# Kernel optimization log

Hardware: AMD Instinct MI355X
Metric: run time of the kernel (lower is better)

Reference implementation:

```python
import jax, jax.numpy as jnp
import numpy as np

N_HEAD = 8
N_QP = 4  # query/key points per head
N_VP = 4  # value points per head
D_SPH = 16  # scalar dims per head
SCALE_SCALAR = D_SPH ** (-0.5)
SCALE_POINT = (4.5 * N_QP) ** (-0.5)
SCALE_TOTAL = 3.0 ** (-0.5)  # scalar + pair bias + point logits


def _euclid(xp, r, t):
    # xp: (b,n,l,p,3), r: (b,l,3,3), t: (b,l,3)  -> row-vector convention: x @ r + t
    return jnp.einsum('bnlpk,blkc->bnlpc', xp, r) + t[:, None, :, None, :]


def _inv_euclid(xp, r, t):
    # (x - t) @ r^T
    return jnp.einsum('bnlpk,blck->bnlpc', xp - t[:, None, :, None, :], r)


def setup_inputs() -> dict:
    key = jax.random.key(0)
    ks = jax.random.split(key, 16)
    b, l, d_res, d_pair = 2, 512, 384, 128
    w = lambda k, shp, fan: jax.random.normal(k, shp, jnp.float32) * (fan ** -0.5)
    return {
        'x': jax.random.normal(ks[0], (b, l, d_res), jnp.float32),
        'e': jax.random.normal(ks[1], (b, l, l, d_pair), jnp.float32),
        'r': jax.random.normal(ks[2], (b, l, 3, 3), jnp.float32),
        't': jax.random.normal(ks[3], (b, l, 3), jnp.float32),
        'Wq_s': w(ks[4], (d_res, N_HEAD * D_SPH), d_res),
        'Wk_s': w(ks[5], (d_res, N_HEAD * D_SPH), d_res),
        'Wv_s': w(ks[6], (d_res, N_HEAD * D_SPH), d_res),
        'Wpb': w(ks[7], (d_pair, N_HEAD), d_pair),
        'Wq_p': w(ks[8], (d_res, N_HEAD * N_QP * 3), d_res),
        'Wk_p': w(ks[9], (d_res, N_HEAD * N_QP * 3), d_res),
        'Wv_p': w(ks[10], (d_res, N_HEAD * N_VP * 3), d_res),
        'gamma': jnp.log(jnp.expm1(jnp.ones((N_HEAD,), jnp.float32))),
        'Wout': w(ks[11], (N_HEAD * D_SPH + N_HEAD * d_pair + N_HEAD * N_VP * 3 + N_HEAD * N_VP, d_res), 1280),
        'bout': jnp.zeros((d_res,), jnp.float32),
    }


def reference(x, e, r, t, Wq_s, Wk_s, Wv_s, Wpb, Wq_p, Wk_p, Wv_p, gamma, Wout, bout):
    b, l, _ = x.shape
    n = N_HEAD

    def split_heads(v):  # (b,l,n*d) -> (b,n,l,d)
        return v.reshape(b, l, n, -1).transpose(0, 2, 1, 3)

    def split_points(v, p):  # (b,l,n*p*3) -> (b,n,l,p,3)
        return v.reshape(b, l, n, p, 3).transpose(0, 2, 1, 3, 4)

    q_s, k_s, v_s = (split_heads(x @ W) for W in (Wq_s, Wk_s, Wv_s))
    q_p = _euclid(split_points(x @ Wq_p, N_QP), r, t)
    k_p = _euclid(split_points(x @ Wk_p, N_QP), r, t)
    v_p = _euclid(split_points(x @ Wv_p, N_VP), r, t)

    logit_scalar = jnp.einsum('bnid,bnjd->bnij', q_s, k_s) * SCALE_SCALAR
    bias_pair = (e @ Wpb).transpose(0, 3, 1, 2)  # (b,n,i,j)
    # pairwise squared point distances, summed over points p and coords c
    diff = q_p[:, :, :, None] - k_p[:, :, None]  # (b,n,i,j,p,3)
    sqdist = (diff ** 2).sum(axis=(-1, -2))      # (b,n,i,j)
    logit_point = -0.5 * SCALE_POINT * gamma[None, :, None, None] * sqdist

    attn = jax.nn.softmax(SCALE_TOTAL * (logit_scalar + bias_pair + logit_point), axis=-1)

    out_scalar = jnp.einsum('bnij,bnjd->bnid', attn, v_s).transpose(0, 2, 1, 3).reshape(b, l, -1)
    out_pair = jnp.einsum('bnij,bijd->bnid', attn, e).transpose(0, 2, 1, 3).reshape(b, l, -1)
    out_point = jnp.einsum('bnij,bnjpc->bnipc', attn, v_p)
    out_point = _inv_euclid(out_point, r, t)  # (b,n,i,p,3)
    out_point_norm = jnp.sqrt((out_point ** 2).sum(-1))  # (b,n,i,p)
    out_point = out_point.transpose(0, 2, 1, 3, 4).reshape(b, l, -1)
    out_point_norm = out_point_norm.transpose(0, 2, 1, 3).reshape(b, l, -1)

    out = jnp.concatenate([out_scalar, out_pair, out_point, out_point_norm], axis=-1)
    return out @ Wout + bout
```

## Files before the change

kernel.cpp:

```cpp
#include <hip/hip_runtime.h>
#include <hip/hip_bf16.h>
#include <math.h>

#define NH 8
#define L 512
#define DP 128
#define DS 16
#define DCAT 1280
#define TJ 32
#define NCHUNK 4
#define CJ 128
#define PSTRIDE 1280

#define SCALE_SCALAR 0.25f
#define SCALE_POINT  0.23570226039551584f
#define SCALE_TOTAL  0.5773502691896258f

typedef __bf16 bf16_t;
typedef bf16_t bf16x8 __attribute__((ext_vector_type(8)));
typedef float  f32x4v __attribute__((ext_vector_type(4)));

__global__ __launch_bounds__(256) void k_pack(
    const float* __restrict__ x,
    const float* __restrict__ Wq_s, const float* __restrict__ Wk_s, const float* __restrict__ Wv_s,
    const float* __restrict__ Wq_p, const float* __restrict__ Wk_p, const float* __restrict__ Wv_p,
    __hip_bfloat16* __restrict__ xb, __hip_bfloat16* __restrict__ WallT) {
    int idx = blockIdx.x * 256 + threadIdx.x;
    const int T1 = 1024 * 384;
    if (idx < T1) {
        xb[idx] = __float2bfloat16(x[idx]);
    } else {
        int j = idx - T1;
        int n = j / 384, k = j % 384;
        float v;
        if      (n < 128) v = Wq_s[k * 128 + n];
        else if (n < 256) v = Wk_s[k * 128 + (n - 128)];
        else if (n < 384) v = Wv_s[k * 128 + (n - 256)];
        else if (n < 480) v = Wq_p[k * 96  + (n - 384)];
        else if (n < 576) v = Wk_p[k * 96  + (n - 480)];
        else              v = Wv_p[k * 96  + (n - 576)];
        WallT[(size_t)n * 384 + k] = __float2bfloat16(v);
    }
}

__global__ __launch_bounds__(256) void k_prep(const float* __restrict__ Wout,
                                              __hip_bfloat16* __restrict__ WoutT) {
    __shared__ float tile[64][65];
    const int tid = threadIdx.x;
    const int k0 = blockIdx.x * 64;
    const int n0 = blockIdx.y * 64;
#pragma unroll
    for (int s = 0; s < 16; ++s) {
        int idx = s * 256 + tid, kk = idx >> 6, nn = idx & 63;
        tile[kk][nn] = Wout[(size_t)(k0 + kk) * 384 + n0 + nn];
    }
    __syncthreads();
#pragma unroll
    for (int s = 0; s < 16; ++s) {
        int idx = s * 256 + tid, nn = idx >> 6, kk = idx & 63;
        WoutT[(size_t)(n0 + nn) * 1280 + k0 + kk] = __float2bfloat16(tile[kk][nn]);
    }
}

__global__ __launch_bounds__(256) void k_projm(
    const __hip_bfloat16* __restrict__ xb, const __hip_bfloat16* __restrict__ WallT,
    float* __restrict__ q_s, float* __restrict__ k_s, float* __restrict__ v_s,
    float* __restrict__ praw) {
    __shared__ __align__(16) bf16_t As[64 * 40];
    __shared__ __align__(16) bf16_t Bs[48 * 40];
    const int tid = threadIdx.x;
    const int row0 = blockIdx.x * 64, col0 = blockIdx.y * 48;
    const int w = tid >> 6, lane = tid & 63;
    f32x4v acc[3] = {};

    for (int k0 = 0; k0 < 384; k0 += 32) {
        __syncthreads();
        {
            int rr = tid >> 2, q = tid & 3;
            *reinterpret_cast<int4*>(&As[rr * 40 + q * 8]) =
                *reinterpret_cast<const int4*>(&xb[(size_t)(row0 + rr) * 384 + k0 + q * 8]);
            if (tid < 192)
                *reinterpret_cast<int4*>(&Bs[rr * 40 + q * 8]) =
                    *reinterpret_cast<const int4*>(&WallT[(size_t)(col0 + rr) * 384 + k0 + q * 8]);
        }
        __syncthreads();
        const int m = lane & 15, kq = lane >> 4;
        bf16x8 af = *reinterpret_cast<const bf16x8*>(&As[(w * 16 + m) * 40 + kq * 8]);
#pragma unroll
        for (int c = 0; c < 3; ++c) {
            bf16x8 bfr = *reinterpret_cast<const bf16x8*>(&Bs[(c * 16 + m) * 40 + kq * 8]);
            acc[c] = __builtin_amdgcn_mfma_f32_16x16x32_bf16(af, bfr, acc[c], 0, 0, 0);
        }
    }
    const int colL = lane & 15, rbase = (lane >> 4) * 4;
#pragma unroll
    for (int c = 0; c < 3; ++c) {
        int col = col0 + c * 16 + colL;
#pragma unroll
        for (int rg = 0; rg < 4; ++rg) {
            int row = row0 + w * 16 + rbase + rg;
            float v = acc[c][rg];
            int bb = row >> 9, ll = row & 511;
            if (col < 384) {
                int kind = col >> 7, n = (col >> 4) & 7, d = col & 15;
                float* dst = (kind == 0) ? q_s : (kind == 1) ? k_s : v_s;
                dst[((size_t)(bb * NH + n) * L + ll) * DS + d] = v;
            } else {
                praw[(size_t)row * 288 + (col - 384)] = v;
            }
        }
    }
}

__global__ __launch_bounds__(256) void k_euclid(
    const float* __restrict__ praw, const float* __restrict__ r, const float* __restrict__ t,
    float* __restrict__ q_p, float* __restrict__ k_p, float* __restrict__ v_p) {
    int idx = blockIdx.x * 256 + threadIdx.x;
    int row = idx / 288, o = idx % 288;
    int arr = o / 96, oo = o % 96;
    int n = oo / 12, pc = oo % 12, p = pc / 3, c = pc % 3;
    const float* base = praw + (size_t)row * 288 + arr * 96 + n * 12 + p * 3;
    float acc = t[row * 3 + c];
#pragma unroll
    for (int k = 0; k < 3; ++k) acc += base[k] * r[row * 9 + k * 3 + c];
    float* dst = (arr == 0) ? q_p : (arr == 1) ? k_p : v_p;
    int bb = row >> 9, ll = row & 511;
    dst[((size_t)(bb * NH + n) * L + ll) * 12 + pc] = acc;
}

__global__ __launch_bounds__(256) void k_attn(
    const float* __restrict__ e, const float* __restrict__ Wpb, const float* __restrict__ gamma,
    const float* __restrict__ q_s, const float* __restrict__ k_s, const float* __restrict__ v_s,
    const float* __restrict__ q_p, const float* __restrict__ k_p, const float* __restrict__ v_p,
    float* __restrict__ part) {
    __shared__ __align__(16) float et[TJ * DP];
    __shared__ __align__(16) float wpbT[NH * DP];
    __shared__ float pt[NH][36];
    __shared__ float ptT[TJ][NH];
    __shared__ __align__(16) float qsl[NH * 16];
    __shared__ __align__(16) float qpl[NH * 12];
    __shared__ float gsh[NH];

    const int tid = threadIdx.x;
    const int blk = blockIdx.x;
    const int bi = blk >> 2, chunk = blk & 3;
    const int b = bi >> 9, i = bi & 511, b8 = b * NH;
    const int nH = tid >> 5, jL = tid & 31;
    const int d4 = tid & 31, jsub = tid >> 5;

    for (int idx = tid; idx < NH * DP; idx += 256)
        wpbT[(idx >> 7) * DP + (idx & 127)] = Wpb[(idx & 127) * NH + (idx >> 7)];
    if (tid < 128) {
        int n = tid >> 4, d = tid & 15;
        qsl[n * 16 + d] = q_s[((size_t)(b8 + n) * L + i) * DS + d];
    } else if (tid < 224) {
        int o = tid - 128, n = o / 12, pc = o % 12;
        qpl[n * 12 + pc] = q_p[((size_t)(b8 + n) * L + i) * 12 + pc];
    } else if (tid < 232) {
        gsh[tid - 224] = gamma[tid - 224];
    }

    const int nS = tid >> 4, dS = tid & 15;
    const int oP = tid - 128;
    const int nP = (oP >= 0 && oP < 96) ? oP / 12 : 0;
    const int pcP = (oP >= 0 && oP < 96) ? oP % 12 : 0;
    const float* vsp = v_s + (((size_t)(b8 + nS) * L + chunk * CJ) << 4) + dS;
    const float* vpp = v_p + ((size_t)(b8 + nP) * L + chunk * CJ) * 12 + pcP;

    float lsum = 0.f;
    float4 accPair[NH];
#pragma unroll
    for (int n = 0; n < NH; ++n) accPair[n] = make_float4(0.f, 0.f, 0.f, 0.f);
    float accS = 0.f, accP = 0.f;

    const float4* esrc4 = reinterpret_cast<const float4*>(
        e + ((size_t)(b * L + i) * L + chunk * CJ) * DP);

    for (int tile = 0; tile < CJ / TJ; ++tile) {
        const int j0 = tile * TJ;
        __syncthreads();
#pragma unroll
        for (int s = 0; s < 4; ++s) {
            int idx = tid + s * 256;
            int j = idx >> 5, g = idx & 31;
            float4 v = esrc4[(size_t)(j0 + j) * 32 + g];
            reinterpret_cast<float4*>(et)[j * 32 + (g ^ j)] = v;
        }
        __syncthreads();
        {
            const int jg = chunk * CJ + j0 + jL;
            const float4* row4 = reinterpret_cast<const float4*>(et) + jL * 32;
            const float4* wr4 = reinterpret_cast<const float4*>(&wpbT[nH * DP]);
            float bsum = 0.f;
#pragma unroll 8
            for (int g = 0; g < 32; ++g) {
                float4 ev = row4[g ^ jL];
                float4 wv4 = wr4[g];
                bsum += ev.x * wv4.x + ev.y * wv4.y + ev.z * wv4.z + ev.w * wv4.w;
            }
            const float4* ksr = reinterpret_cast<const float4*>(k_s + (((size_t)(b8 + nH) * L + jg) << 4));
            const float4* q4 = reinterpret_cast<const float4*>(&qsl[nH * 16]);
            float ssum = 0.f;
#pragma unroll
            for (int g = 0; g < 4; ++g) {
                float4 kv = ksr[g], qv = q4[g];
                ssum += kv.x * qv.x + kv.y * qv.y + kv.z * qv.z + kv.w * qv.w;
            }
            const float4* kpr = reinterpret_cast<const float4*>(k_p + ((size_t)(b8 + nH) * L + jg) * 12);
            const float4* qp4 = reinterpret_cast<const float4*>(&qpl[nH * 12]);
            float sq = 0.f;
#pragma unroll
            for (int g = 0; g < 3; ++g) {
                float4 kv = kpr[g], qv = qp4[g];
                float d0;
                d0 = qv.x - kv.x; sq += d0 * d0;  d0 = qv.y - kv.y; sq += d0 * d0;
                d0 = qv.z - kv.z; sq += d0 * d0;  d0 = qv.w - kv.w; sq += d0 * d0;
            }
            float lg = SCALE_TOTAL * (ssum * SCALE_SCALAR + bsum
                                      - 0.5f * SCALE_POINT * gsh[nH] * sq);
            float pv = __expf(lg);
            lsum += pv;
            pt[nH][jL] = pv;
            ptT[jL][nH] = pv;
        }
        __syncthreads();
        {
            const float4* et4 = reinterpret_cast<const float4*>(et);
#pragma unroll
            for (int s = 0; s < 4; ++s) {
                int j = jsub * 4 + s;
                float4 ev = et4[j * 32 + (d4 ^ j)];
                const float4* pb4 = reinterpret_cast<const float4*>(&ptT[j][0]);
                float4 pA = pb4[0], pB = pb4[1];
#define ACCP(nn, ps) accPair[nn].x += (ps) * ev.x; accPair[nn].y += (ps) * ev.y; \
                     accPair[nn].z += (ps) * ev.z; accPair[nn].w += (ps) * ev.w;
                ACCP(0, pA.x) ACCP(1, pA.y) ACCP(2, pA.z) ACCP(3, pA.w)
                ACCP(4, pB.x) ACCP(5, pB.y) ACCP(6, pB.z) ACCP(7, pB.w)
#undef ACCP
            }
        }
        if (tid < 128) {
            const float* vp = vsp + (size_t)j0 * 16;
#pragma unroll
            for (int q = 0; q < 8; ++q) {
                float4 p4 = *reinterpret_cast<const float4*>(&pt[nS][q * 4]);
                accS += p4.x * vp[(q * 4 + 0) * 16] + p4.y * vp[(q * 4 + 1) * 16]
                      + p4.z * vp[(q * 4 + 2) * 16] + p4.w * vp[(q * 4 + 3) * 16];
            }
        } else if (tid < 224) {
            const float* vp = vpp + (size_t)j0 * 12;
#pragma unroll
            for (int q = 0; q < 8; ++q) {
                float4 p4 = *reinterpret_cast<const float4*>(&pt[nP][q * 4]);
                accP += p4.x * vp[(q * 4 + 0) * 12] + p4.y * vp[(q * 4 + 1) * 12]
                      + p4.z * vp[(q * 4 + 2) * 12] + p4.w * vp[(q * 4 + 3) * 12];
            }
        }
    }

    float* prow = part + (size_t)blk * PSTRIDE;
    lsum += __shfl_xor(lsum, 1);  lsum += __shfl_xor(lsum, 2);
    lsum += __shfl_xor(lsum, 4);  lsum += __shfl_xor(lsum, 8);
    lsum += __shfl_xor(lsum, 16);
    if (jL == 0) prow[1248 + nH] = lsum;
    if (tid < 128) prow[1024 + tid] = accS;
    else if (tid < 224) prow[1152 + (tid - 128)] = accP;

    float4* red4 = reinterpret_cast<float4*>(et);
    __syncthreads();
    if (jsub >= 4) {
#pragma unroll
        for (int n = 0; n < NH; ++n) red4[((jsub - 4) * NH + n) * 32 + d4] = accPair[n];
    }
    __syncthreads();
    if (jsub < 4) {
#pragma unroll
        for (int n = 0; n < NH; ++n) {
            float4 o = red4[(jsub * NH + n) * 32 + d4];
            accPair[n].x += o.x; accPair[n].y += o.y; accPair[n].z += o.z; accPair[n].w += o.w;
        }
    }
    __syncthreads();
    if (jsub == 2 || jsub == 3) {
#pragma unroll
        for (int n = 0; n < NH; ++n) red4[((jsub - 2) * NH + n) * 32 + d4] = accPair[n];
    }
    __syncthreads();
    if (jsub < 2) {
#pragma unroll
        for (int n = 0; n < NH; ++n) {
            float4 o = red4[(jsub * NH + n) * 32 + d4];
            accPair[n].x += o.x; accPair[n].y += o.y; accPair[n].z += o.z; accPair[n].w += o.w;
        }
    }
    __syncthreads();
    if (jsub == 1) {
#pragma unroll
        for (int n = 0; n < NH; ++n) red4[n * 32 + d4] = accPair[n];
    }
    __syncthreads();
    if (jsub == 0) {
#pragma unroll
        for (int n = 0; n < NH; ++n) {
            float4 o = red4[n * 32 + d4];
            accPair[n].x += o.x; accPair[n].y += o.y; accPair[n].z += o.z; accPair[n].w += o.w;
            *reinterpret_cast<float4*>(&prow[n * 128 + d4 * 4]) = accPair[n];
        }
    }
}

__global__ __launch_bounds__(256) void k_comb(
    const float* __restrict__ part, const float* __restrict__ r, const float* __restrict__ t,
    __hip_bfloat16* __restrict__ concat) {
    __shared__ float comb[1256];
    __shared__ float rtsh[12], osh[96], o2sh[96];
    const int tid = threadIdx.x;
    const int bi = blockIdx.x;
    const float* base = part + (size_t)bi * NCHUNK * PSTRIDE;
#pragma unroll
    for (int s = 0; s < 5; ++s) {
        int idx = tid + s * 256;
        if (idx < 1256)
            comb[idx] = base[idx] + base[PSTRIDE + idx] + base[2 * PSTRIDE + idx] + base[3 * PSTRIDE + idx];
    }
    if (tid >= 244 && tid < 256) {
        int c = tid - 244;
        rtsh[c] = (c < 9) ? r[bi * 9 + c] : t[bi * 3 + (c - 9)];
    }
    __syncthreads();
    __hip_bfloat16* crow = concat + (size_t)bi * DCAT;
    if (tid < 128) crow[tid] = __float2bfloat16(comb[1024 + tid] / comb[1248 + (tid >> 4)]);
    for (int idx = tid; idx < 1024; idx += 256)
        crow[128 + idx] = __float2bfloat16(comb[idx] / comb[1248 + (idx >> 7)]);
    if (tid >= 128 && tid < 224) {
        int o = tid - 128;
        osh[o] = comb[1152 + o] / comb[1248 + o / 12];
    }
    __syncthreads();
    if (tid < 96) {
        int n = tid / 12, pc = tid % 12, p = pc / 3, c = pc % 3;
        float oc = 0.f;
#pragma unroll
        for (int k = 0; k < 3; ++k)
            oc += (osh[n * 12 + p * 3 + k] - rtsh[9 + k]) * rtsh[c * 3 + k];
        crow[1152 + tid] = __float2bfloat16(oc);
        o2sh[tid] = oc;
    }
    __syncthreads();
    if (tid < 32) {
        int n = tid >> 2, p = tid & 3;
        float vx = o2sh[n * 12 + p * 3], vy = o2sh[n * 12 + p * 3 + 1], vz = o2sh[n * 12 + p * 3 + 2];
        crow[1248 + tid] = __float2bfloat16(sqrtf(vx * vx + vy * vy + vz * vz));
    }
}

__global__ __launch_bounds__(256) void k_out(const __hip_bfloat16* __restrict__ A,
                                             const __hip_bfloat16* __restrict__ Bt,
                                             const float* __restrict__ bout,
                                             float* __restrict__ out) {
    __shared__ __align__(16) bf16_t At[64 * 40];
    __shared__ __align__(16) bf16_t Bs[64 * 40];
    const int tid = threadIdx.x;
    const int row0 = blockIdx.x * 64, col0 = blockIdx.y * 64;
    const int wv = tid >> 6, lane = tid & 63;
    f32x4v acc[4] = {};

    for (int k0 = 0; k0 < 1280; k0 += 32) {
        __syncthreads();
        {
            int rr = tid >> 2, q = tid & 3;
            *reinterpret_cast<int4*>(&At[rr * 40 + q * 8]) =
                *reinterpret_cast<const int4*>(&A[(size_t)(row0 + rr) * 1280 + k0 + q * 8]);
            *reinterpret_cast<int4*>(&Bs[rr * 40 + q * 8]) =
                *reinterpret_cast<const int4*>(&Bt[(size_t)(col0 + rr) * 1280 + k0 + q * 8]);
        }
        __syncthreads();
        const int m = lane & 15, kq = lane >> 4;
        bf16x8 af = *reinterpret_cast<const bf16x8*>(&At[(wv * 16 + m) * 40 + kq * 8]);
#pragma unroll
        for (int nt = 0; nt < 4; ++nt) {
            bf16x8 bfr = *reinterpret_cast<const bf16x8*>(&Bs[(nt * 16 + m) * 40 + kq * 8]);
            acc[nt] = __builtin_amdgcn_mfma_f32_16x16x32_bf16(af, bfr, acc[nt], 0, 0, 0);
        }
    }
    const int col_l = lane & 15, rbase = (lane >> 4) * 4;
#pragma unroll
    for (int nt = 0; nt < 4; ++nt) {
        int col = col0 + nt * 16 + col_l;
        float bo = bout[col];
#pragma unroll
        for (int rg = 0; rg < 4; ++rg) {
            int rowg = row0 + wv * 16 + rbase + rg;
            out[(size_t)rowg * 384 + col] = acc[nt][rg] + bo;
        }
    }
}

extern "C" void kernel_launch(void* const* d_in, const int* in_sizes, int n_in,
                              void* d_out, int out_size, void* d_ws, size_t ws_size,
                              hipStream_t stream) {
    const float* x     = (const float*)d_in[0];
    const float* e     = (const float*)d_in[1];
    const float* r     = (const float*)d_in[2];
    const float* t     = (const float*)d_in[3];
    const float* Wq_s  = (const float*)d_in[4];
    const float* Wk_s  = (const float*)d_in[5];
    const float* Wv_s  = (const float*)d_in[6];
    const float* Wpb   = (const float*)d_in[7];
    const float* Wq_p  = (const float*)d_in[8];
    const float* Wk_p  = (const float*)d_in[9];
    const float* Wv_p  = (const float*)d_in[10];
    const float* gamma = (const float*)d_in[11];
    const float* Wout  = (const float*)d_in[12];
    const float* bout  = (const float*)d_in[13];

    float* ws   = (float*)d_ws;
    float* q_s  = ws + 0;
    float* k_s  = ws + 131072;
    float* v_s  = ws + 262144;
    float* q_p  = ws + 393216;
    float* k_p  = ws + 491520;
    float* v_p  = ws + 589824;
    float* praw = ws + 688128;
    __hip_bfloat16* xb     = (__hip_bfloat16*)((char*)d_ws + 3932160);
    __hip_bfloat16* WallT  = (__hip_bfloat16*)((char*)d_ws + 4718592);
    __hip_bfloat16* concat = (__hip_bfloat16*)((char*)d_ws + 5234688);
    __hip_bfloat16* WoutT  = (__hip_bfloat16*)((char*)d_ws + 7856128);
    float* part = (float*)((char*)d_ws + 8847360);
    float* out = (float*)d_out;

    hipLaunchKernelGGL(k_pack, dim3(2544), dim3(256), 0, stream,
                       x, Wq_s, Wk_s, Wv_s, Wq_p, Wk_p, Wv_p, xb, WallT);
    hipLaunchKernelGGL(k_prep, dim3(20, 6), dim3(256), 0, stream, Wout, WoutT);
    hipLaunchKernelGGL(k_projm, dim3(16, 14), dim3(256), 0, stream,
                       xb, WallT, q_s, k_s, v_s, praw);
    hipLaunchKernelGGL(k_euclid, dim3(1152), dim3(256), 0, stream,
                       praw, r, t, q_p, k_p, v_p);
    hipLaunchKernelGGL(k_attn, dim3(4096), dim3(256), 0, stream,
                       e, Wpb, gamma, q_s, k_s, v_s, q_p, k_p, v_p, part);
    hipLaunchKernelGGL(k_comb, dim3(1024), dim3(256), 0, stream,
                       part, r, t, concat);
    hipLaunchKernelGGL(k_out, dim3(16, 6), dim3(256), 0, stream, concat, WoutT, bout, out);
}
```

Measured before the change: 485.7 us.

## Use bf16 MFMA for pair bias and pair aggregation in attention kernel

Rewrites the attention kernel so the e·Wpb pair-bias projection and the attn·e pair aggregation run on 16x16x32 bf16 MFMA instructions. The e tile is converted to bf16 and stored both row-major and transposed in shared memory. The next e tile is prefetched into registers, and V scalars and points are read from new transposed bf16 copies written by the projection kernels. This removes the scalar FMA loops and the multi-stage shared-memory reduction of the pair accumulators, at the cost of bf16 precision on e, the probabilities and V, plus extra transposed writes.

```diff
diff --git a/kernel.cpp b/kernel.cpp
--- a/kernel.cpp
+++ b/kernel.cpp
@@ -18,6 +18,7 @@
 
 typedef __bf16 bf16_t;
 typedef bf16_t bf16x8 __attribute__((ext_vector_type(8)));
+typedef bf16_t bf16x4 __attribute__((ext_vector_type(4)));
 typedef float  f32x4v __attribute__((ext_vector_type(4)));
 
 __global__ __launch_bounds__(256) void k_pack(
@@ -65,7 +66,7 @@
 __global__ __launch_bounds__(256) void k_projm(
     const __hip_bfloat16* __restrict__ xb, const __hip_bfloat16* __restrict__ WallT,
     float* __restrict__ q_s, float* __restrict__ k_s, float* __restrict__ v_s,
-    float* __restrict__ praw) {
+    float* __restrict__ praw, __hip_bfloat16* __restrict__ v_sT) {
     __shared__ __align__(16) bf16_t As[64 * 40];
     __shared__ __align__(16) bf16_t Bs[48 * 40];
     const int tid = threadIdx.x;
@@ -105,6 +106,8 @@
                 int kind = col >> 7, n = (col >> 4) & 7, d = col & 15;
                 float* dst = (kind == 0) ? q_s : (kind == 1) ? k_s : v_s;
                 dst[((size_t)(bb * NH + n) * L + ll) * DS + d] = v;
+                if (kind == 2)
+                    v_sT[((size_t)((bb * NH + n) * DS + d)) * L + ll] = __float2bfloat16(v);
             } else {
                 praw[(size_t)row * 288 + (col - 384)] = v;
             }
@@ -114,7 +117,8 @@
 
 __global__ __launch_bounds__(256) void k_euclid(
     const float* __restrict__ praw, const float* __restrict__ r, const float* __restrict__ t,
-    float* __restrict__ q_p, float* __restrict__ k_p, float* __restrict__ v_p) {
+    float* __restrict__ q_p, float* __restrict__ k_p, float* __restrict__ v_p,
+    __hip_bfloat16* __restrict__ v_pT) {
     int idx = blockIdx.x * 256 + threadIdx.x;
     int row = idx / 288, o = idx % 288;
     int arr = o / 96, oo = o % 96;
@@ -126,30 +130,32 @@
     float* dst = (arr == 0) ? q_p : (arr == 1) ? k_p : v_p;
     int bb = row >> 9, ll = row & 511;
     dst[((size_t)(bb * NH + n) * L + ll) * 12 + pc] = acc;
-}
-
-__global__ __launch_bounds__(256) void k_attn(
+    if (arr == 2)
+        v_pT[((size_t)((bb * NH + n) * 12 + pc)) * L + ll] = __float2bfloat16(acc);
+}
+
+__global__ __launch_bounds__(256, 4) void k_attn(
     const float* __restrict__ e, const float* __restrict__ Wpb, const float* __restrict__ gamma,
-    const float* __restrict__ q_s, const float* __restrict__ k_s, const float* __restrict__ v_s,
-    const float* __restrict__ q_p, const float* __restrict__ k_p, const float* __restrict__ v_p,
+    const float* __restrict__ q_s, const float* __restrict__ k_s,
+    const float* __restrict__ q_p, const float* __restrict__ k_p,
+    const __hip_bfloat16* __restrict__ v_sT, const __hip_bfloat16* __restrict__ v_pT,
     float* __restrict__ part) {
-    __shared__ __align__(16) float et[TJ * DP];
-    __shared__ __align__(16) float wpbT[NH * DP];
-    __shared__ float pt[NH][36];
-    __shared__ float ptT[TJ][NH];
+    __shared__ __align__(16) bf16_t etA[TJ * 136];
+    __shared__ __align__(16) bf16_t etB[DP * 40];
+    __shared__ __align__(16) bf16_t pT[16 * 40];
+    __shared__ __align__(16) float pt32[NH * 36];
     __shared__ __align__(16) float qsl[NH * 16];
     __shared__ __align__(16) float qpl[NH * 12];
-    __shared__ float gsh[NH];
+    __shared__ float csh[NH];
+    __shared__ float lsumw[16];
 
     const int tid = threadIdx.x;
     const int blk = blockIdx.x;
     const int bi = blk >> 2, chunk = blk & 3;
     const int b = bi >> 9, i = bi & 511, b8 = b * NH;
-    const int nH = tid >> 5, jL = tid & 31;
-    const int d4 = tid & 31, jsub = tid >> 5;
-
-    for (int idx = tid; idx < NH * DP; idx += 256)
-        wpbT[(idx >> 7) * DP + (idx & 127)] = Wpb[(idx & 127) * NH + (idx >> 7)];
+    const int w = tid >> 6, lane = tid & 63;
+    const int c15 = lane & 15, quad = lane >> 4;
+
     if (tid < 128) {
         int n = tid >> 4, d = tid & 15;
         qsl[n * 16 + d] = q_s[((size_t)(b8 + n) * L + i) * DS + d];
@@ -157,156 +163,163 @@
         int o = tid - 128, n = o / 12, pc = o % 12;
         qpl[n * 12 + pc] = q_p[((size_t)(b8 + n) * L + i) * 12 + pc];
     } else if (tid < 232) {
-        gsh[tid - 224] = gamma[tid - 224];
-    }
-
-    const int nS = tid >> 4, dS = tid & 15;
-    const int oP = tid - 128;
-    const int nP = (oP >= 0 && oP < 96) ? oP / 12 : 0;
-    const int pcP = (oP >= 0 && oP < 96) ? oP % 12 : 0;
-    const float* vsp = v_s + (((size_t)(b8 + nS) * L + chunk * CJ) << 4) + dS;
-    const float* vpp = v_p + ((size_t)(b8 + nP) * L + chunk * CJ) * 12 + pcP;
-
-    float lsum = 0.f;
-    float4 accPair[NH];
-#pragma unroll
-    for (int n = 0; n < NH; ++n) accPair[n] = make_float4(0.f, 0.f, 0.f, 0.f);
-    float accS = 0.f, accP = 0.f;
+        int n = tid - 224;
+        csh[n] = SCALE_TOTAL * 0.5f * SCALE_POINT * gamma[n];
+    }
+    bf16x8 wpbF[4];
+#pragma unroll
+    for (int ks = 0; ks < 4; ++ks)
+#pragma unroll
+        for (int ii = 0; ii < 8; ++ii) {
+            int d = ks * 32 + quad * 8 + ii;
+            float wv = (c15 < 8) ? Wpb[d * NH + c15] : 0.f;
+            wpbF[ks][ii] = (bf16_t)(SCALE_TOTAL * wv);
+        }
 
     const float4* esrc4 = reinterpret_cast<const float4*>(
         e + ((size_t)(b * L + i) * L + chunk * CJ) * DP);
 
-    for (int tile = 0; tile < CJ / TJ; ++tile) {
-        const int j0 = tile * TJ;
+    float4 pre[4];
+#pragma unroll
+    for (int s = 0; s < 4; ++s) {
+        int idx = tid + s * 256, j = idx >> 5, g = idx & 31;
+        pre[s] = esrc4[(size_t)j * 32 + g];
+    }
+
+    f32x4v accP[2] = {};
+    float accS = 0.f, accP3 = 0.f, lsum = 0.f;
+    const int tid2 = tid - 128;
+    const int nS = (tid2 >= 0) ? (tid2 >> 4) : 0, dS = (tid2 >= 0) ? (tid2 & 15) : 0;
+    const int nP = (tid2 >= 0 && tid2 < 96) ? tid2 / 12 : 0;
+    const int pcP = (tid2 >= 0 && tid2 < 96) ? tid2 % 12 : 0;
+    const __hip_bfloat16* vsp = v_sT + ((size_t)((b8 + nS) * DS + dS)) * L + chunk * CJ;
+    const __hip_bfloat16* vpp = v_pT + ((size_t)((b8 + nP) * 12 + pcP)) * L + chunk * CJ;
+
+    for (int tt = 0; tt < CJ / TJ; ++tt) {
         __syncthreads();
 #pragma unroll
         for (int s = 0; s < 4; ++s) {
-            int idx = tid + s * 256;
-            int j = idx >> 5, g = idx & 31;
-            float4 v = esrc4[(size_t)(j0 + j) * 32 + g];
-            reinterpret_cast<float4*>(et)[j * 32 + (g ^ j)] = v;
+            int idx = tid + s * 256, j = idx >> 5, g = idx & 31;
+            float4 v = pre[s];
+            bf16x4 a;
+            a[0] = (bf16_t)v.x; a[1] = (bf16_t)v.y; a[2] = (bf16_t)v.z; a[3] = (bf16_t)v.w;
+            *reinterpret_cast<bf16x4*>(&etA[j * 136 + 4 * g]) = a;
+            etB[(4 * g + 0) * 40 + j] = a[0];
+            etB[(4 * g + 1) * 40 + j] = a[1];
+            etB[(4 * g + 2) * 40 + j] = a[2];
+            etB[(4 * g + 3) * 40 + j] = a[3];
+        }
+        if (tt < CJ / TJ - 1) {
+#pragma unroll
+            for (int s = 0; s < 4; ++s) {
+                int idx = tid + s * 256, j = idx >> 5, g = idx & 31;
+                pre[s] = esrc4[(size_t)(tt + 1) * TJ * 32 + (size_t)j * 32 + g];
+            }
+        }
+        __syncthreads();
+        if (w < 2) {
+            f32x4v bc = {};
+#pragma unroll
+            for (int ks = 0; ks < 4; ++ks) {
+                bf16x8 af = *reinterpret_cast<const bf16x8*>(
+                    &etA[(w * 16 + c15) * 136 + ks * 32 + quad * 8]);
+                bc = __builtin_amdgcn_mfma_f32_16x16x32_bf16(af, wpbF[ks], bc, 0, 0, 0);
+            }
+            const int n = c15;
+#pragma unroll
+            for (int r = 0; r < 4; ++r) {
+                int jl = w * 16 + quad * 4 + r;
+                float pv = 0.f;
+                if (n < 8) {
+                    int jg = chunk * CJ + tt * TJ + jl;
+                    const float4* ksr = reinterpret_cast<const float4*>(
+                        k_s + (((size_t)(b8 + n) * L + jg) << 4));
+                    const float4* q4 = reinterpret_cast<const float4*>(&qsl[n * 16]);
+                    float ss = 0.f;
+#pragma unroll
+                    for (int g = 0; g < 4; ++g) {
+                        float4 kv = ksr[g], qv = q4[g];
+                        ss += kv.x * qv.x + kv.y * qv.y + kv.z * qv.z + kv.w * qv.w;
+                    }
+                    const float4* kpr = reinterpret_cast<const float4*>(
+                        k_p + ((size_t)(b8 + n) * L + jg) * 12);
+                    const float4* qp4 = reinterpret_cast<const float4*>(&qpl[n * 12]);
+                    float sq = 0.f;
+#pragma unroll
+                    for (int g = 0; g < 3; ++g) {
+                        float4 kv = kpr[g], qv = qp4[g];
+                        float d0;
+                        d0 = qv.x - kv.x; sq += d0 * d0;  d0 = qv.y - kv.y; sq += d0 * d0;
+                        d0 = qv.z - kv.z; sq += d0 * d0;  d0 = qv.w - kv.w; sq += d0 * d0;
+                    }
+                    float lg = bc[r] + (SCALE_TOTAL * SCALE_SCALAR) * ss - csh[n] * sq;
+                    pv = __expf(lg);
+                    pt32[n * 36 + jl] = pv;
+                }
+                lsum += pv;
+                pT[n * 40 + jl] = (bf16_t)pv;
+            }
         }
         __syncthreads();
         {
-            const int jg = chunk * CJ + j0 + jL;
-            const float4* row4 = reinterpret_cast<const float4*>(et) + jL * 32;
-            const float4* wr4 = reinterpret_cast<const float4*>(&wpbT[nH * DP]);
-            float bsum = 0.f;
-#pragma unroll 8
-            for (int g = 0; g < 32; ++g) {
-                float4 ev = row4[g ^ jL];
-                float4 wv4 = wr4[g];
-                bsum += ev.x * wv4.x + ev.y * wv4.y + ev.z * wv4.z + ev.w * wv4.w;
-            }
-            const float4* ksr = reinterpret_cast<const float4*>(k_s + (((size_t)(b8 + nH) * L + jg) << 4));
-            const float4* q4 = reinterpret_cast<const float4*>(&qsl[nH * 16]);
-            float ssum = 0.f;
-#pragma unroll
-            for (int g = 0; g < 4; ++g) {
-                float4 kv = ksr[g], qv = q4[g];
-                ssum += kv.x * qv.x + kv.y * qv.y + kv.z * qv.z + kv.w * qv.w;
-            }
-            const float4* kpr = reinterpret_cast<const float4*>(k_p + ((size_t)(b8 + nH) * L + jg) * 12);
-            const float4* qp4 = reinterpret_cast<const float4*>(&qpl[nH * 12]);
-            float sq = 0.f;
-#pragma unroll
-            for (int g = 0; g < 3; ++g) {
-                float4 kv = kpr[g], qv = qp4[g];
-                float d0;
-                d0 = qv.x - kv.x; sq += d0 * d0;  d0 = qv.y - kv.y; sq += d0 * d0;
-                d0 = qv.z - kv.z; sq += d0 * d0;  d0 = qv.w - kv.w; sq += d0 * d0;
-            }
-            float lg = SCALE_TOTAL * (ssum * SCALE_SCALAR + bsum
-                                      - 0.5f * SCALE_POINT * gsh[nH] * sq);
-            float pv = __expf(lg);
-            lsum += pv;
-            pt[nH][jL] = pv;
-            ptT[jL][nH] = pv;
-        }
-        __syncthreads();
-        {
-            const float4* et4 = reinterpret_cast<const float4*>(et);
-#pragma unroll
-            for (int s = 0; s < 4; ++s) {
-                int j = jsub * 4 + s;
-                float4 ev = et4[j * 32 + (d4 ^ j)];
-                const float4* pb4 = reinterpret_cast<const float4*>(&ptT[j][0]);
-                float4 pA = pb4[0], pB = pb4[1];
-#define ACCP(nn, ps) accPair[nn].x += (ps) * ev.x; accPair[nn].y += (ps) * ev.y; \
-                     accPair[nn].z += (ps) * ev.z; accPair[nn].w += (ps) * ev.w;
-                ACCP(0, pA.x) ACCP(1, pA.y) ACCP(2, pA.z) ACCP(3, pA.w)
-                ACCP(4, pB.x) ACCP(5, pB.y) ACCP(6, pB.z) ACCP(7, pB.w)
-#undef ACCP
-            }
-        }
-        if (tid < 128) {
-            const float* vp = vsp + (size_t)j0 * 16;
-#pragma unroll
-            for (int q = 0; q < 8; ++q) {
-                float4 p4 = *reinterpret_cast<const float4*>(&pt[nS][q * 4]);
-                accS += p4.x * vp[(q * 4 + 0) * 16] + p4.y * vp[(q * 4 + 1) * 16]
-                      + p4.z * vp[(q * 4 + 2) * 16] + p4.w * vp[(q * 4 + 3) * 16];
-            }
-        } else if (tid < 224) {
-            const float* vp = vpp + (size_t)j0 * 12;
-#pragma unroll
-            for (int q = 0; q < 8; ++q) {
-                float4 p4 = *reinterpret_cast<const float4*>(&pt[nP][q * 4]);
-                accP += p4.x * vp[(q * 4 + 0) * 12] + p4.y * vp[(q * 4 + 1) * 12]
-                      + p4.z * vp[(q * 4 + 2) * 12] + p4.w * vp[(q * 4 + 3) * 12];
-            }
-        }
-    }
+            bf16x8 ap = *reinterpret_cast<const bf16x8*>(&pT[c15 * 40 + quad * 8]);
+#pragma unroll
+            for (int tb = 0; tb < 2; ++tb) {
+                int d = (w * 2 + tb) * 16 + c15;
+                bf16x8 bfr = *reinterpret_cast<const bf16x8*>(&etB[d * 40 + quad * 8]);
+                accP[tb] = __builtin_amdgcn_mfma_f32_16x16x32_bf16(ap, bfr, accP[tb], 0, 0, 0);
+            }
+        }
+        if (w >= 2) {
+            {
+                const __hip_bfloat16* vp = vsp + tt * TJ;
+#pragma unroll
+                for (int q = 0; q < 4; ++q) {
+                    bf16x8 vv = *reinterpret_cast<const bf16x8*>(vp + q * 8);
+                    float4 pA = *reinterpret_cast<const float4*>(&pt32[nS * 36 + q * 8]);
+                    float4 pB = *reinterpret_cast<const float4*>(&pt32[nS * 36 + q * 8 + 4]);
+                    accS += pA.x * (float)vv[0] + pA.y * (float)vv[1]
+                          + pA.z * (float)vv[2] + pA.w * (float)vv[3]
+                          + pB.x * (float)vv[4] + pB.y * (float)vv[5]
+                          + pB.z * (float)vv[6] + pB.w * (float)vv[7];
+                }
+            }
+            if (tid2 < 96) {
+                const __hip_bfloat16* vp = vpp + tt * TJ;
+#pragma unroll
+                for (int q = 0; q < 4; ++q) {
+                    bf16x8 vv = *reinterpret_cast<const bf16x8*>(vp + q * 8);
+                    float4 pA = *reinterpret_cast<const float4*>(&pt32[nP * 36 + q * 8]);
+                    float4 pB = *reinterpret_cast<const float4*>(&pt32[nP * 36 + q * 8 + 4]);
+                    accP3 += pA.x * (float)vv[0] + pA.y * (float)vv[1]
+                           + pA.z * (float)vv[2] + pA.w * (float)vv[3]
+                           + pB.x * (float)vv[4] + pB.y * (float)vv[5]
+                           + pB.z * (float)vv[6] + pB.w * (float)vv[7];
+                }
+            }
+        }
+    }
+
+    lsum += __shfl_xor(lsum, 16);
+    lsum += __shfl_xor(lsum, 32);
+    if (w < 2 && lane < 8) lsumw[w * 8 + lane] = lsum;
+    __syncthreads();
 
     float* prow = part + (size_t)blk * PSTRIDE;
-    lsum += __shfl_xor(lsum, 1);  lsum += __shfl_xor(lsum, 2);
-    lsum += __shfl_xor(lsum, 4);  lsum += __shfl_xor(lsum, 8);
-    lsum += __shfl_xor(lsum, 16);
-    if (jL == 0) prow[1248 + nH] = lsum;
-    if (tid < 128) prow[1024 + tid] = accS;
-    else if (tid < 224) prow[1152 + (tid - 128)] = accP;
-
-    float4* red4 = reinterpret_cast<float4*>(et);
-    __syncthreads();
-    if (jsub >= 4) {
-#pragma unroll
-        for (int n = 0; n < NH; ++n) red4[((jsub - 4) * NH + n) * 32 + d4] = accPair[n];
-    }
-    __syncthreads();
-    if (jsub < 4) {
-#pragma unroll
-        for (int n = 0; n < NH; ++n) {
-            float4 o = red4[(jsub * NH + n) * 32 + d4];
-            accPair[n].x += o.x; accPair[n].y += o.y; accPair[n].z += o.z; accPair[n].w += o.w;
-        }
-    }
-    __syncthreads();
-    if (jsub == 2 || jsub == 3) {
-#pragma unroll
-        for (int n = 0; n < NH; ++n) red4[((jsub - 2) * NH + n) * 32 + d4] = accPair[n];
-    }
-    __syncthreads();
-    if (jsub < 2) {
-#pragma unroll
-        for (int n = 0; n < NH; ++n) {
-            float4 o = red4[(jsub * NH + n) * 32 + d4];
-            accPair[n].x += o.x; accPair[n].y += o.y; accPair[n].z += o.z; accPair[n].w += o.w;
-        }
-    }
-    __syncthreads();
-    if (jsub == 1) {
-#pragma unroll
-        for (int n = 0; n < NH; ++n) red4[n * 32 + d4] = accPair[n];
-    }
-    __syncthreads();
-    if (jsub == 0) {
-#pragma unroll
-        for (int n = 0; n < NH; ++n) {
-            float4 o = red4[n * 32 + d4];
-            accPair[n].x += o.x; accPair[n].y += o.y; accPair[n].z += o.z; accPair[n].w += o.w;
-            *reinterpret_cast<float4*>(&prow[n * 128 + d4 * 4]) = accPair[n];
-        }
-    }
+    if (w >= 2) {
+        prow[1024 + tid2] = accS;
+        if (tid2 < 96) prow[1152 + tid2] = accP3;
+    }
+    if (quad < 2) {
+#pragma unroll
+        for (int tb = 0; tb < 2; ++tb)
+#pragma unroll
+            for (int r = 0; r < 4; ++r) {
+                int h = quad * 4 + r;
+                prow[h * 128 + (w * 2 + tb) * 16 + c15] = accP[tb][r];
+            }
+    }
+    if (tid < 8) prow[1248 + tid] = lsumw[tid] + lsumw[8 + tid];
 }
 
 __global__ __launch_bounds__(256) void k_comb(
@@ -427,17 +440,19 @@
     __hip_bfloat16* concat = (__hip_bfloat16*)((char*)d_ws + 5234688);
     __hip_bfloat16* WoutT  = (__hip_bfloat16*)((char*)d_ws + 7856128);
     float* part = (float*)((char*)d_ws + 8847360);
+    __hip_bfloat16* v_sT = (__hip_bfloat16*)((char*)d_ws + 29818880);
+    __hip_bfloat16* v_pT = (__hip_bfloat16*)((char*)d_ws + 30081024);
     float* out = (float*)d_out;
 
     hipLaunchKernelGGL(k_pack, dim3(2544), dim3(256), 0, stream,
                        x, Wq_s, Wk_s, Wv_s, Wq_p, Wk_p, Wv_p, xb, WallT);
     hipLaunchKernelGGL(k_prep, dim3(20, 6), dim3(256), 0, stream, Wout, WoutT);
     hipLaunchKernelGGL(k_projm, dim3(16, 14), dim3(256), 0, stream,
-                       xb, WallT, q_s, k_s, v_s, praw);
+                       xb, WallT, q_s, k_s, v_s, praw, v_sT);
     hipLaunchKernelGGL(k_euclid, dim3(1152), dim3(256), 0, stream,
-                       praw, r, t, q_p, k_p, v_p);
+                       praw, r, t, q_p, k_p, v_p, v_pT);
     hipLaunchKernelGGL(k_attn, dim3(4096), dim3(256), 0, stream,
-                       e, Wpb, gamma, q_s, k_s, v_s, q_p, k_p, v_p, part);
+                       e, Wpb, gamma, q_s, k_s, q_p, k_p, v_sT, v_pT, part);
     hipLaunchKernelGGL(k_comb, dim3(1024), dim3(256), 0, stream,
                        part, r, t, concat);
     hipLaunchKernelGGL(k_out, dim3(16, 6), dim3(256), 0, stream, concat, WoutT, bout, out);
```

Result: slower. 579.1 us (+19.2%).
